# Kernel optimization log

Hardware: AMD Instinct MI355X
Metric: run time of the kernel (lower is better)

The kernel has to match this reference:

```python
import jax, jax.numpy as jnp
import numpy as np
import math

B, S, DM, H, D = 2, 2048, 768, 12, 64
MAX_POS = 2048

def setup_inputs() -> dict:
    key = jax.random.key(0)
    ks = jax.random.split(key, 8)
    return {
        "hidden_states": jax.random.normal(ks[0], (B, S, DM), jnp.float32),
        "attention_mask": jnp.zeros((B, 1, 1, S), jnp.float32),
        "Wq": jax.random.normal(ks[1], (DM, DM), jnp.float32) * 0.02,
        "bq": jnp.zeros((DM,), jnp.float32),
        "Wk": jax.random.normal(ks[2], (DM, DM), jnp.float32) * 0.02,
        "bk": jnp.zeros((DM,), jnp.float32),
        "Wv": jax.random.normal(ks[3], (DM, DM), jnp.float32) * 0.02,
        "bv": jnp.zeros((DM,), jnp.float32),
        "dist_emb": jax.random.normal(ks[4], (2 * MAX_POS - 1, D), jnp.float32) * 0.02,
    }

def reference(hidden_states, attention_mask, Wq, bq, Wk, bk, Wv, bv, dist_emb):
    def heads(x):  # [B,S,DM] -> [B,H,S,D]
        return x.reshape(B, S, H, D).transpose(0, 2, 1, 3)
    q = heads(hidden_states @ Wq + bq)
    k = heads(hidden_states @ Wk + bk)
    v = heads(hidden_states @ Wv + bv)
    scores = jnp.einsum("bhqd,bhkd->bhqk", q, k)  # [B,H,S,S]
    # relative_key_query position bias
    pos = jnp.arange(S)
    distance = pos[:, None] - pos[None, :] + (MAX_POS - 1)  # [S,S]
    pe = dist_emb[distance]  # [S,S,D]
    scores = scores + jnp.einsum("bhld,lrd->bhlr", q, pe) + jnp.einsum("bhrd,lrd->bhlr", k, pe)
    scores = scores / math.sqrt(D) + attention_mask
    probs = jax.nn.softmax(scores, axis=-1)
    ctx = jnp.einsum("bhqk,bhkd->bhqd", probs, v)
    return ctx.transpose(0, 2, 1, 3).reshape(B, S, DM)
```

## Files before the change

kernel.cpp:

```cpp
#include <hip/hip_runtime.h>
#include <hip/hip_fp16.h>

#define NB 2
#define NS 2048
#define NDM 768
#define NH 12
#define ND 64

typedef __attribute__((ext_vector_type(8))) _Float16 f16x8;
typedef __attribute__((ext_vector_type(4))) float f32x4;

__device__ __forceinline__ int swz(int row) {
  return (row & 3) ^ ((row >> 2) & 3);
}

__launch_bounds__(256)
__global__ void cvt_split(const float* __restrict__ x, __half* __restrict__ xh,
                          __half* __restrict__ xl) {
  const int i = blockIdx.x * 256 + threadIdx.x;
  const float4 v = reinterpret_cast<const float4*>(x)[i];
  const float a[4] = {v.x, v.y, v.z, v.w};
  union { __half h[4]; uint2 u; } ph, pl;
#pragma unroll
  for (int j = 0; j < 4; ++j) {
    ph.h[j] = __float2half(a[j]);
    pl.h[j] = __float2half(a[j] - __half2float(ph.h[j]));
  }
  *reinterpret_cast<uint2*>(&xh[(size_t)i * 4]) = ph.u;
  *reinterpret_cast<uint2*>(&xl[(size_t)i * 4]) = pl.u;
}

__launch_bounds__(256)
__global__ void cvt_w_t(const float* __restrict__ Wq,
                        const float* __restrict__ Wk,
                        const float* __restrict__ Wv,
                        __half* __restrict__ WhT, __half* __restrict__ WlT) {
  __shared__ float Tf[64][65];
  const int t = threadIdx.x;
  const int k0 = blockIdx.x * 64;
  const int n0 = blockIdx.y * 64;
  const int z = blockIdx.z;
  const float* W = z == 0 ? Wq : (z == 1 ? Wk : Wv);
  __half* wh = WhT + (size_t)z * NDM * NDM;
  __half* wl = WlT + (size_t)z * NDM * NDM;
#pragma unroll
  for (int s = 0; s < 4; ++s) {
    const int lin = t + 256 * s;
    const int r = lin >> 4, c4 = (lin & 15) * 4;
    const float4 v = *reinterpret_cast<const float4*>(
        &W[(size_t)(k0 + r) * NDM + n0 + c4]);
    Tf[r][c4 + 0] = v.x;
    Tf[r][c4 + 1] = v.y;
    Tf[r][c4 + 2] = v.z;
    Tf[r][c4 + 3] = v.w;
  }
  __syncthreads();
#pragma unroll
  for (int s = 0; s < 4; ++s) {
    const int lin = t + 256 * s;
    const int nl = lin >> 4, k4 = (lin & 15) * 4;
    union { __half h[4]; uint2 u; } ph, pl;
#pragma unroll
    for (int i = 0; i < 4; ++i) {
      const float f = Tf[k4 + i][nl];
      ph.h[i] = __float2half(f);
      pl.h[i] = __float2half(f - __half2float(ph.h[i]));
    }
    *reinterpret_cast<uint2*>(&wh[(size_t)(n0 + nl) * NDM + k0 + k4]) = ph.u;
    *reinterpret_cast<uint2*>(&wl[(size_t)(n0 + nl) * NDM + k0 + k4]) = pl.u;
  }
}

__launch_bounds__(256, 2)
__global__ void qkv_mfma(const __half* __restrict__ Xh,
                         const __half* __restrict__ Xl,
                         const __half* __restrict__ WhT,
                         const __half* __restrict__ WlT,
                         const float* __restrict__ bq,
                         const float* __restrict__ bk,
                         const float* __restrict__ bv,
                         __half* __restrict__ qb, __half* __restrict__ kb,
                         __half* __restrict__ vb) {
  __shared__ __align__(16) __half SS[4][128 * 32];

  const int t = threadIdx.x;
  const int lane = t & 63;
  const int w = t >> 6;
  const int g = lane >> 4;
  const int L = lane & 15;
  const int wm = w & 1, wn = w >> 1;
  const int widx = blockIdx.x / 6;
  const int n0m = (blockIdx.x % 6) * 128;
  const int m0 = blockIdx.y * 128;

  const __half* wh = WhT + (size_t)widx * NDM * NDM;
  const __half* wl = WlT + (size_t)widx * NDM * NDM;
  const float* bias = widx == 0 ? bq : (widx == 1 ? bk : bv);
  __half* dst = widx == 0 ? qb : (widx == 1 ? kb : vb);

  const __half* srcs[4] = {Xh + (size_t)m0 * NDM, Xl + (size_t)m0 * NDM,
                           wh + (size_t)n0m * NDM, wl + (size_t)n0m * NDM};

  uint4 rv[8];
#pragma unroll
  for (int u = 0; u < 8; ++u) {
    const int slot = t + 256 * u;
    const int bsel = slot >> 9, within = slot & 511;
    const int row = within >> 2, blk = within & 3;
    rv[u] = *reinterpret_cast<const uint4*>(srcs[bsel] + (size_t)row * NDM +
                                            blk * 8);
  }

  f32x4 acc[4][4];
#pragma unroll
  for (int mt = 0; mt < 4; ++mt)
#pragma unroll
    for (int nt = 0; nt < 4; ++nt) acc[mt][nt] = {0.f, 0.f, 0.f, 0.f};

  const int sL = (L & 3) ^ ((L >> 2) & 3);
  const int gs = (g ^ sL) << 3;

  for (int kt = 0; kt < 24; ++kt) {
    __syncthreads();
#pragma unroll
    for (int u = 0; u < 8; ++u) {
      const int slot = t + 256 * u;
      const int bsel = slot >> 9, within = slot & 511;
      const int row = within >> 2, blk = within & 3;
      *reinterpret_cast<uint4*>(&SS[bsel][row * 32 + ((blk ^ swz(row)) << 3)]) =
          rv[u];
    }
    if (kt < 23) {
      const int k0 = (kt + 1) * 32;
#pragma unroll
      for (int u = 0; u < 8; ++u) {
        const int slot = t + 256 * u;
        const int bsel = slot >> 9, within = slot & 511;
        const int row = within >> 2, blk = within & 3;
        rv[u] = *reinterpret_cast<const uint4*>(
            srcs[bsel] + (size_t)row * NDM + k0 + blk * 8);
      }
    }
    __syncthreads();

    f16x8 bh[4], bl[4];
#pragma unroll
    for (int nt = 0; nt < 4; ++nt) {
      const int nl = 64 * wn + 16 * nt + L;
      bh[nt] = *reinterpret_cast<const f16x8*>(&SS[2][nl * 32 + gs]);
      bl[nt] = *reinterpret_cast<const f16x8*>(&SS[3][nl * 32 + gs]);
    }
#pragma unroll
    for (int mt = 0; mt < 4; ++mt) {
      const int ml = 64 * wm + 16 * mt + L;
      const f16x8 ah = *reinterpret_cast<const f16x8*>(&SS[0][ml * 32 + gs]);
      const f16x8 al = *reinterpret_cast<const f16x8*>(&SS[1][ml * 32 + gs]);
#pragma unroll
      for (int nt = 0; nt < 4; ++nt) {
        acc[mt][nt] =
            __builtin_amdgcn_mfma_f32_16x16x32_f16(al, bh[nt], acc[mt][nt], 0, 0, 0);
        acc[mt][nt] =
            __builtin_amdgcn_mfma_f32_16x16x32_f16(ah, bl[nt], acc[mt][nt], 0, 0, 0);
        acc[mt][nt] =
            __builtin_amdgcn_mfma_f32_16x16x32_f16(ah, bh[nt], acc[mt][nt], 0, 0, 0);
      }
    }
  }

#pragma unroll
  for (int nt = 0; nt < 4; ++nt) {
    const int nmat = n0m + 64 * wn + 16 * nt + L;
    const float bval = bias[nmat];
    const int h_ = nmat >> 6, d_ = nmat & 63;
#pragma unroll
    for (int mt = 0; mt < 4; ++mt) {
#pragma unroll
      for (int j = 0; j < 4; ++j) {
        const int m = m0 + 64 * wm + 16 * mt + 4 * g + j;
        const int b_ = m >> 11, s_ = m & (NS - 1);
        dst[(((size_t)b_ * NH + h_) * NS + s_) * ND + d_] =
            __float2half(acc[mt][nt][j] + bval);
      }
    }
  }
}

__launch_bounds__(256, 3)
__global__ void attn_mfma(const __half* __restrict__ q,
                          const __half* __restrict__ k,
                          const __half* __restrict__ v,
                          const float* __restrict__ E,
                          const float* __restrict__ mask,
                          float* __restrict__ out) {
  __shared__ __align__(16) __half Qs[64 * 64];
  __shared__ __align__(16) __half Ks[32 * 64];
  __shared__ __align__(16) __half Es[96 * 64];
  __shared__ __align__(16) __half Vt[64 * 40];
  __shared__ __half F1s[64 * 100];
  __shared__ __half F2s[32 * 100];
  __shared__ __align__(16) __half Ps[64 * 40];

  const int t    = threadIdx.x;
  const int lane = t & 63;
  const int w    = t >> 6;
  const int g    = lane >> 4;
  const int L    = lane & 15;
  const int l0   = blockIdx.x * 64;
  const int bh   = blockIdx.y;
  const int b    = bh / NH;
  const int h    = bh - b * NH;

  const __half* qp = q + ((size_t)bh * NS + l0) * ND;
  const __half* kp = k + (size_t)bh * NS * ND;
  const __half* vp = v + (size_t)bh * NS * ND;
  const float* mp = mask + (size_t)b * NS;

#pragma unroll
  for (int s = 0; s < 4; ++s) {
    const int tau = t + 256 * s;
    const int r = tau >> 4, qd = tau & 15;
    const uint2 val =
        *reinterpret_cast<const uint2*>(&qp[(size_t)r * ND + qd * 4]);
    const int idx = r * 64 + ((((qd >> 1) ^ (r & 7)) << 3) | ((qd & 1) << 2));
    *reinterpret_cast<uint2*>(&Qs[idx]) = val;
  }

  f32x4 Oacc[4];
  float m_run[4], l_run[4];
#pragma unroll
  for (int j = 0; j < 4; ++j) { m_run[j] = -1e30f; l_run[j] = 0.f; }
#pragma unroll
  for (int nt = 0; nt < 4; ++nt) Oacc[nt] = {0.f, 0.f, 0.f, 0.f};

  const int rtw    = w >> 1;
  const int dtbase = (w & 1) * 3;
  const int swL    = L & 7;
  const f32x4 Z = {0.f, 0.f, 0.f, 0.f};

  for (int r0 = 0; r0 < NS; r0 += 32) {
    __syncthreads();

#pragma unroll
    for (int s = 0; s < 2; ++s) {
      const int tau = t + 256 * s;
      const int r = tau >> 4, qd = tau & 15;
      const uint2 val = *reinterpret_cast<const uint2*>(
          &kp[(size_t)(r0 + r) * ND + qd * 4]);
      const int idx =
          r * 64 + ((((qd >> 1) ^ (r & 7)) << 3) | ((qd & 1) << 2));
      *reinterpret_cast<uint2*>(&Ks[idx]) = val;
    }
#pragma unroll
    for (int s = 0; s < 2; ++s) {
      const int tau = t + 256 * s;
      const int rr = tau & 31, qd = tau >> 5;
      union { uint2 u; __half h[4]; } x;
      x.u = *reinterpret_cast<const uint2*>(
          &vp[(size_t)(r0 + rr) * ND + qd * 4]);
      Vt[(qd * 4 + 0) * 40 + rr] = x.h[0];
      Vt[(qd * 4 + 1) * 40 + rr] = x.h[1];
      Vt[(qd * 4 + 2) * 40 + rr] = x.h[2];
      Vt[(qd * 4 + 3) * 40 + rr] = x.h[3];
    }
    const int start = l0 - r0 + 2016;
#pragma unroll
    for (int s = 0; s < 3; ++s) {
      const int tau = t + 256 * s;
      const int row = tau >> 3, blk = tau & 7;
      int grow = start + row;
      grow = grow > 4094 ? 4094 : grow;
      const float* ep = &E[(size_t)grow * ND + blk * 8];
      const float4 a = *reinterpret_cast<const float4*>(ep);
      const float4 c = *reinterpret_cast<const float4*>(ep + 4);
      union { __half2 h2[4]; uint4 u; } pk;
      pk.h2[0] = __floats2half2_rn(a.x, a.y);
      pk.h2[1] = __floats2half2_rn(a.z, a.w);
      pk.h2[2] = __floats2half2_rn(c.x, c.y);
      pk.h2[3] = __floats2half2_rn(c.z, c.w);
      *reinterpret_cast<uint4*>(&Es[row * 64 + ((blk ^ (row & 7)) << 3)]) =
          pk.u;
    }
    __syncthreads();

    const int rq = 16 * w + L;
    const f16x8 aQ0 = *reinterpret_cast<const f16x8*>(
        &Qs[rq * 64 + ((g ^ swL) << 3)]);
    const f16x8 aQ1 = *reinterpret_cast<const f16x8*>(
        &Qs[rq * 64 + (((4 + g) ^ swL) << 3)]);
    const f16x8 bK00 = *reinterpret_cast<const f16x8*>(
        &Ks[L * 64 + ((g ^ swL) << 3)]);
    const f16x8 bK01 = *reinterpret_cast<const f16x8*>(
        &Ks[L * 64 + (((4 + g) ^ swL) << 3)]);
    const f16x8 bK10 = *reinterpret_cast<const f16x8*>(
        &Ks[(16 + L) * 64 + ((g ^ swL) << 3)]);
    const f16x8 bK11 = *reinterpret_cast<const f16x8*>(
        &Ks[(16 + L) * 64 + (((4 + g) ^ swL) << 3)]);

    f32x4 c0 = Z, c1 = Z;
    c0 = __builtin_amdgcn_mfma_f32_16x16x32_f16(aQ0, bK00, c0, 0, 0, 0);
    c0 = __builtin_amdgcn_mfma_f32_16x16x32_f16(aQ1, bK01, c0, 0, 0, 0);
    c1 = __builtin_amdgcn_mfma_f32_16x16x32_f16(aQ0, bK10, c1, 0, 0, 0);
    c1 = __builtin_amdgcn_mfma_f32_16x16x32_f16(aQ1, bK11, c1, 0, 0, 0);

    f32x4 f1acc[6];
#pragma unroll
    for (int dt = 0; dt < 6; ++dt) {
      const int re = 16 * dt + L;
      const f16x8 be0 = *reinterpret_cast<const f16x8*>(
          &Es[re * 64 + ((g ^ swL) << 3)]);
      const f16x8 be1 = *reinterpret_cast<const f16x8*>(
          &Es[re * 64 + (((4 + g) ^ swL) << 3)]);
      f32x4 acc = Z;
      acc = __builtin_amdgcn_mfma_f32_16x16x32_f16(aQ0, be0, acc, 0, 0, 0);
      acc = __builtin_amdgcn_mfma_f32_16x16x32_f16(aQ1, be1, acc, 0, 0, 0);
      f1acc[dt] = acc;
    }
    const f16x8 aK0 = rtw ? bK10 : bK00;
    const f16x8 aK1 = rtw ? bK11 : bK01;
    f32x4 f2acc[3];
#pragma unroll
    for (int m = 0; m < 3; ++m) {
      const int re = 16 * (dtbase + m) + L;
      const f16x8 be0 = *reinterpret_cast<const f16x8*>(
          &Es[re * 64 + ((g ^ swL) << 3)]);
      const f16x8 be1 = *reinterpret_cast<const f16x8*>(
          &Es[re * 64 + (((4 + g) ^ swL) << 3)]);
      f32x4 acc = Z;
      acc = __builtin_amdgcn_mfma_f32_16x16x32_f16(aK0, be0, acc, 0, 0, 0);
      acc = __builtin_amdgcn_mfma_f32_16x16x32_f16(aK1, be1, acc, 0, 0, 0);
      f2acc[m] = acc;
    }

#pragma unroll
    for (int dt = 0; dt < 6; ++dt)
#pragma unroll
      for (int j = 0; j < 4; ++j)
        F1s[(16 * w + 4 * g + j) * 100 + 16 * dt + L] =
            __float2half(f1acc[dt][j]);
#pragma unroll
    for (int m = 0; m < 3; ++m)
#pragma unroll
      for (int j = 0; j < 4; ++j)
        F2s[(16 * rtw + 4 * g + j) * 100 + 16 * (dtbase + m) + L] =
            __float2half(f2acc[m][j]);
    __syncthreads();

    float sc2[2][4];
    const float mk0 = mp[r0 + L];
    const float mk1 = mp[r0 + 16 + L];
#pragma unroll
    for (int j = 0; j < 4; ++j) {
      const int ll = 16 * w + 4 * g + j;
      {
        const int dl = ll - L + 31;
        sc2[0][j] = (c0[j] + __half2float(F1s[ll * 100 + dl]) +
                     __half2float(F2s[L * 100 + dl])) * 0.125f + mk0;
      }
      {
        const int rl = 16 + L;
        const int dl = ll - rl + 31;
        sc2[1][j] = (c1[j] + __half2float(F1s[ll * 100 + dl]) +
                     __half2float(F2s[rl * 100 + dl])) * 0.125f + mk1;
      }
    }
    float al[4];
#pragma unroll
    for (int j = 0; j < 4; ++j) {
      float mx = fmaxf(sc2[0][j], sc2[1][j]);
      mx = fmaxf(mx, __shfl_xor(mx, 1));
      mx = fmaxf(mx, __shfl_xor(mx, 2));
      mx = fmaxf(mx, __shfl_xor(mx, 4));
      mx = fmaxf(mx, __shfl_xor(mx, 8));
      const float mnew = fmaxf(m_run[j], mx);
      al[j] = __expf(m_run[j] - mnew);
      m_run[j] = mnew;
      const float p0 = __expf(sc2[0][j] - mnew);
      const float p1 = __expf(sc2[1][j] - mnew);
      sc2[0][j] = p0;
      sc2[1][j] = p1;
      float ps = p0 + p1;
      ps += __shfl_xor(ps, 1);
      ps += __shfl_xor(ps, 2);
      ps += __shfl_xor(ps, 4);
      ps += __shfl_xor(ps, 8);
      l_run[j] = l_run[j] * al[j] + ps;
    }
#pragma unroll
    for (int nt = 0; nt < 4; ++nt)
#pragma unroll
      for (int j = 0; j < 4; ++j) Oacc[nt][j] *= al[j];
#pragma unroll
    for (int j = 0; j < 4; ++j) {
      Ps[(16 * w + 4 * g + j) * 40 + L]      = __float2half(sc2[0][j]);
      Ps[(16 * w + 4 * g + j) * 40 + 16 + L] = __float2half(sc2[1][j]);
    }
    __syncthreads();

    {
      const f16x8 aP =
          *reinterpret_cast<const f16x8*>(&Ps[(16 * w + L) * 40 + 8 * g]);
#pragma unroll
      for (int nt = 0; nt < 4; ++nt) {
        const f16x8 bV = *reinterpret_cast<const f16x8*>(
            &Vt[(16 * nt + L) * 40 + 8 * g]);
        Oacc[nt] = __builtin_amdgcn_mfma_f32_16x16x32_f16(aP, bV, Oacc[nt],
                                                          0, 0, 0);
      }
    }
  }

#pragma unroll
  for (int j = 0; j < 4; ++j) {
    const float inv = 1.0f / l_run[j];
    const int row = l0 + 16 * w + 4 * g + j;
    float* op = &out[((size_t)b * NS + row) * NDM + h * ND + L];
    op[0]  = Oacc[0][j] * inv;
    op[16] = Oacc[1][j] * inv;
    op[32] = Oacc[2][j] * inv;
    op[48] = Oacc[3][j] * inv;
  }
}

extern "C" void kernel_launch(void* const* d_in, const int* in_sizes, int n_in,
                              void* d_out, int out_size, void* d_ws, size_t ws_size,
                              hipStream_t stream) {
  const float* hs  = (const float*)d_in[0];
  const float* msk = (const float*)d_in[1];
  const float* Wq  = (const float*)d_in[2];
  const float* bq  = (const float*)d_in[3];
  const float* Wk  = (const float*)d_in[4];
  const float* bk  = (const float*)d_in[5];
  const float* Wv  = (const float*)d_in[6];
  const float* bv  = (const float*)d_in[7];
  const float* Ept = (const float*)d_in[8];
  float* out = (float*)d_out;

  const size_t per  = (size_t)NB * NH * NS * ND;
  const size_t wsz  = (size_t)NDM * NDM;
  __half* qb  = (__half*)d_ws;
  __half* kb  = qb + per;
  __half* vb  = kb + per;
  __half* Xh  = vb + per;
  __half* Xl  = Xh + per;
  __half* WhT = Xl + per;
  __half* WlT = WhT + 3 * wsz;

  cvt_split<<<dim3((int)(per / 4 / 256)), 256, 0, stream>>>(hs, Xh, Xl);
  cvt_w_t<<<dim3(12, 12, 3), 256, 0, stream>>>(Wq, Wk, Wv, WhT, WlT);
  qkv_mfma<<<dim3(18, 32), 256, 0, stream>>>(Xh, Xl, WhT, WlT, bq, bk, bv,
                                             qb, kb, vb);
  attn_mfma<<<dim3(NS / 64, NB * NH), 256, 0, stream>>>(qb, kb, vb, Ept,
                                                        msk, out);
}
```

Before: 637.0 us.

## Enlarge attention key tile to 64 with register prefetch and ring-buffered E rows

The attention kernel now processes 64 keys per iteration instead of 32. The next tile's K, V and E rows are prefetched into registers while the current tile computes, and E is kept in a 128-row ring buffer so only 64 new rows load per step. It also computes the full F2 term per wave, adds s_setprio around the MFMA sections, and unions Ks with Ps to save LDS. Occupancy drops from 3 to 2 blocks per SIMD and register pressure rises, traded for fewer barriers per key and better hiding of global loads.

```diff
diff --git a/kernel.cpp b/kernel.cpp
--- a/kernel.cpp
+++ b/kernel.cpp
@@ -185,89 +185,66 @@
   }
 }
 
-__launch_bounds__(256, 3)
+__launch_bounds__(256, 2)
 __global__ void attn_mfma(const __half* __restrict__ q,
                           const __half* __restrict__ k,
                           const __half* __restrict__ v,
                           const float* __restrict__ E,
                           const float* __restrict__ mask,
                           float* __restrict__ out) {
-  __shared__ __align__(16) __half Qs[64 * 64];
-  __shared__ __align__(16) __half Ks[32 * 64];
-  __shared__ __align__(16) __half Es[96 * 64];
-  __shared__ __align__(16) __half Vt[64 * 40];
-  __shared__ __half F1s[64 * 100];
-  __shared__ __half F2s[32 * 100];
-  __shared__ __align__(16) __half Ps[64 * 40];
+  struct __align__(16) SMem {
+    __half Qs[64 * 64];
+    union { __half Ks[64 * 64]; __half Ps[64 * 72]; } kp;
+    __half Es[128 * 64];
+    __half Vt[64 * 72];
+    __half F1[64 * 132];
+    __half F2[64 * 132];
+  };
+  __shared__ SMem sm;
 
   const int t    = threadIdx.x;
   const int lane = t & 63;
   const int w    = t >> 6;
   const int g    = lane >> 4;
   const int L    = lane & 15;
+  const int sw   = L & 7;
   const int l0   = blockIdx.x * 64;
   const int bh   = blockIdx.y;
   const int b    = bh / NH;
   const int h    = bh - b * NH;
 
-  const __half* qp = q + ((size_t)bh * NS + l0) * ND;
-  const __half* kp = k + (size_t)bh * NS * ND;
-  const __half* vp = v + (size_t)bh * NS * ND;
-  const float* mp = mask + (size_t)b * NS;
+  const __half* qp  = q + ((size_t)bh * NS + l0) * ND;
+  const __half* kpg = k + (size_t)bh * NS * ND;
+  const __half* vpg = v + (size_t)bh * NS * ND;
+  const float*  mp  = mask + (size_t)b * NS;
 
 #pragma unroll
   for (int s = 0; s < 4; ++s) {
     const int tau = t + 256 * s;
     const int r = tau >> 4, qd = tau & 15;
-    const uint2 val =
+    const int idx = r * 64 + ((((qd >> 1) ^ (r & 7)) << 3) | ((qd & 1) << 2));
+    sm.Qs[0] = sm.Qs[0];
+    *reinterpret_cast<uint2*>(&sm.Qs[idx]) =
         *reinterpret_cast<const uint2*>(&qp[(size_t)r * ND + qd * 4]);
-    const int idx = r * 64 + ((((qd >> 1) ^ (r & 7)) << 3) | ((qd & 1) << 2));
-    *reinterpret_cast<uint2*>(&Qs[idx]) = val;
-  }
-
-  f32x4 Oacc[4];
-  float m_run[4], l_run[4];
-#pragma unroll
-  for (int j = 0; j < 4; ++j) { m_run[j] = -1e30f; l_run[j] = 0.f; }
-#pragma unroll
-  for (int nt = 0; nt < 4; ++nt) Oacc[nt] = {0.f, 0.f, 0.f, 0.f};
-
-  const int rtw    = w >> 1;
-  const int dtbase = (w & 1) * 3;
-  const int swL    = L & 7;
-  const f32x4 Z = {0.f, 0.f, 0.f, 0.f};
-
-  for (int r0 = 0; r0 < NS; r0 += 32) {
-    __syncthreads();
-
-#pragma unroll
-    for (int s = 0; s < 2; ++s) {
-      const int tau = t + 256 * s;
-      const int r = tau >> 4, qd = tau & 15;
-      const uint2 val = *reinterpret_cast<const uint2*>(
-          &kp[(size_t)(r0 + r) * ND + qd * 4]);
-      const int idx =
-          r * 64 + ((((qd >> 1) ^ (r & 7)) << 3) | ((qd & 1) << 2));
-      *reinterpret_cast<uint2*>(&Ks[idx]) = val;
-    }
-#pragma unroll
-    for (int s = 0; s < 2; ++s) {
-      const int tau = t + 256 * s;
-      const int rr = tau & 31, qd = tau >> 5;
-      union { uint2 u; __half h[4]; } x;
-      x.u = *reinterpret_cast<const uint2*>(
-          &vp[(size_t)(r0 + rr) * ND + qd * 4]);
-      Vt[(qd * 4 + 0) * 40 + rr] = x.h[0];
-      Vt[(qd * 4 + 1) * 40 + rr] = x.h[1];
-      Vt[(qd * 4 + 2) * 40 + rr] = x.h[2];
-      Vt[(qd * 4 + 3) * 40 + rr] = x.h[3];
-    }
-    const int start = l0 - r0 + 2016;
-#pragma unroll
-    for (int s = 0; s < 3; ++s) {
+    *reinterpret_cast<uint2*>(&sm.kp.Ks[idx]) =
+        *reinterpret_cast<const uint2*>(&kpg[(size_t)r * ND + qd * 4]);
+  }
+#pragma unroll
+  for (int s = 0; s < 4; ++s) {
+    const int tau = t + 256 * s;
+    const int rr = tau & 63, qd = tau >> 6;
+    union { uint2 u; __half hh[4]; } x;
+    x.u = *reinterpret_cast<const uint2*>(&vpg[(size_t)rr * ND + qd * 4]);
+#pragma unroll
+    for (int c = 0; c < 4; ++c) sm.Vt[(qd * 4 + c) * 72 + rr] = x.hh[c];
+  }
+  {
+    const int start0 = l0 + 1984;
+#pragma unroll
+    for (int s = 0; s < 4; ++s) {
       const int tau = t + 256 * s;
       const int row = tau >> 3, blk = tau & 7;
-      int grow = start + row;
+      int grow = start0 + row;
       grow = grow > 4094 ? 4094 : grow;
       const float* ep = &E[(size_t)grow * ND + blk * 8];
       const float4 a = *reinterpret_cast<const float4*>(ep);
@@ -277,96 +254,118 @@
       pk.h2[1] = __floats2half2_rn(a.z, a.w);
       pk.h2[2] = __floats2half2_rn(c.x, c.y);
       pk.h2[3] = __floats2half2_rn(c.z, c.w);
-      *reinterpret_cast<uint4*>(&Es[row * 64 + ((blk ^ (row & 7)) << 3)]) =
+      *reinterpret_cast<uint4*>(&sm.Es[row * 64 + ((blk ^ (row & 7)) << 3)]) =
           pk.u;
     }
+  }
+  __syncthreads();
+
+  const int rq = 16 * w + L;
+  const f16x8 aQ0 =
+      *reinterpret_cast<const f16x8*>(&sm.Qs[rq * 64 + ((g ^ sw) << 3)]);
+  const f16x8 aQ1 =
+      *reinterpret_cast<const f16x8*>(&sm.Qs[rq * 64 + (((4 + g) ^ sw) << 3)]);
+
+  f32x4 Oacc[4];
+  float m_run[4], l_run[4];
+#pragma unroll
+  for (int j = 0; j < 4; ++j) { m_run[j] = -1e30f; l_run[j] = 0.f; }
+#pragma unroll
+  for (int nt = 0; nt < 4; ++nt) Oacc[nt] = {0.f, 0.f, 0.f, 0.f};
+
+  const f32x4 Z = {0.f, 0.f, 0.f, 0.f};
+
+  for (int it = 0; it < 32; ++it) {
+    const int r0 = it * 64;
+    const int off = (it & 1) * 64;
+
+    uint2 kr[4], vr[4];
+    float4 er[4];
+    const bool pf = it < 31;
+    if (pf) {
+      const int r0n = r0 + 64;
+#pragma unroll
+      for (int s = 0; s < 4; ++s) {
+        const int tau = t + 256 * s;
+        kr[s] = *reinterpret_cast<const uint2*>(
+            &kpg[(size_t)(r0n + (tau >> 4)) * ND + (tau & 15) * 4]);
+        vr[s] = *reinterpret_cast<const uint2*>(
+            &vpg[(size_t)(r0n + (tau & 63)) * ND + (tau >> 6) * 4]);
+      }
+      const int startn = l0 + 1984 - 64 * (it + 1);
+#pragma unroll
+      for (int s = 0; s < 2; ++s) {
+        const int tau = t + 256 * s;
+        const int row = tau >> 3, blk = tau & 7;
+        const float* ep = &E[(size_t)(startn + row) * ND + blk * 8];
+        er[2 * s]     = *reinterpret_cast<const float4*>(ep);
+        er[2 * s + 1] = *reinterpret_cast<const float4*>(ep + 4);
+      }
+    }
+    float mk[4];
+#pragma unroll
+    for (int rt = 0; rt < 4; ++rt) mk[rt] = mp[r0 + 16 * rt + L];
+
+    __builtin_amdgcn_s_setprio(1);
+    f16x8 bKa[4], bKb[4];
+#pragma unroll
+    for (int rt = 0; rt < 4; ++rt) {
+      const int rl = 16 * rt + L;
+      bKa[rt] = *reinterpret_cast<const f16x8*>(
+          &sm.kp.Ks[rl * 64 + ((g ^ sw) << 3)]);
+      bKb[rt] = *reinterpret_cast<const f16x8*>(
+          &sm.kp.Ks[rl * 64 + (((4 + g) ^ sw) << 3)]);
+    }
+    f32x4 c[4];
+#pragma unroll
+    for (int rt = 0; rt < 4; ++rt) {
+      f32x4 acc = Z;
+      acc = __builtin_amdgcn_mfma_f32_16x16x32_f16(aQ0, bKa[rt], acc, 0, 0, 0);
+      acc = __builtin_amdgcn_mfma_f32_16x16x32_f16(aQ1, bKb[rt], acc, 0, 0, 0);
+      c[rt] = acc;
+    }
+    const f16x8 aK0 = *reinterpret_cast<const f16x8*>(
+        &sm.kp.Ks[(16 * w + L) * 64 + ((g ^ sw) << 3)]);
+    const f16x8 aK1 = *reinterpret_cast<const f16x8*>(
+        &sm.kp.Ks[(16 * w + L) * 64 + (((4 + g) ^ sw) << 3)]);
+#pragma unroll
+    for (int dt = 0; dt < 8; ++dt) {
+      const int phys = ((16 * dt + L) + off) & 127;
+      const f16x8 be0 = *reinterpret_cast<const f16x8*>(
+          &sm.Es[phys * 64 + ((g ^ sw) << 3)]);
+      const f16x8 be1 = *reinterpret_cast<const f16x8*>(
+          &sm.Es[phys * 64 + (((4 + g) ^ sw) << 3)]);
+      f32x4 f1 = Z, f2 = Z;
+      f1 = __builtin_amdgcn_mfma_f32_16x16x32_f16(aQ0, be0, f1, 0, 0, 0);
+      f1 = __builtin_amdgcn_mfma_f32_16x16x32_f16(aQ1, be1, f1, 0, 0, 0);
+      f2 = __builtin_amdgcn_mfma_f32_16x16x32_f16(aK0, be0, f2, 0, 0, 0);
+      f2 = __builtin_amdgcn_mfma_f32_16x16x32_f16(aK1, be1, f2, 0, 0, 0);
+#pragma unroll
+      for (int j = 0; j < 4; ++j) {
+        const int rowi = 16 * w + 4 * g + j;
+        sm.F1[rowi * 132 + 16 * dt + L] = __float2half(f1[j]);
+        sm.F2[rowi * 132 + 16 * dt + L] = __float2half(f2[j]);
+      }
+    }
+    __builtin_amdgcn_s_setprio(0);
     __syncthreads();
 
-    const int rq = 16 * w + L;
-    const f16x8 aQ0 = *reinterpret_cast<const f16x8*>(
-        &Qs[rq * 64 + ((g ^ swL) << 3)]);
-    const f16x8 aQ1 = *reinterpret_cast<const f16x8*>(
-        &Qs[rq * 64 + (((4 + g) ^ swL) << 3)]);
-    const f16x8 bK00 = *reinterpret_cast<const f16x8*>(
-        &Ks[L * 64 + ((g ^ swL) << 3)]);
-    const f16x8 bK01 = *reinterpret_cast<const f16x8*>(
-        &Ks[L * 64 + (((4 + g) ^ swL) << 3)]);
-    const f16x8 bK10 = *reinterpret_cast<const f16x8*>(
-        &Ks[(16 + L) * 64 + ((g ^ swL) << 3)]);
-    const f16x8 bK11 = *reinterpret_cast<const f16x8*>(
-        &Ks[(16 + L) * 64 + (((4 + g) ^ swL) << 3)]);
-
-    f32x4 c0 = Z, c1 = Z;
-    c0 = __builtin_amdgcn_mfma_f32_16x16x32_f16(aQ0, bK00, c0, 0, 0, 0);
-    c0 = __builtin_amdgcn_mfma_f32_16x16x32_f16(aQ1, bK01, c0, 0, 0, 0);
-    c1 = __builtin_amdgcn_mfma_f32_16x16x32_f16(aQ0, bK10, c1, 0, 0, 0);
-    c1 = __builtin_amdgcn_mfma_f32_16x16x32_f16(aQ1, bK11, c1, 0, 0, 0);
-
-    f32x4 f1acc[6];
-#pragma unroll
-    for (int dt = 0; dt < 6; ++dt) {
-      const int re = 16 * dt + L;
-      const f16x8 be0 = *reinterpret_cast<const f16x8*>(
-          &Es[re * 64 + ((g ^ swL) << 3)]);
-      const f16x8 be1 = *reinterpret_cast<const f16x8*>(
-          &Es[re * 64 + (((4 + g) ^ swL) << 3)]);
-      f32x4 acc = Z;
-      acc = __builtin_amdgcn_mfma_f32_16x16x32_f16(aQ0, be0, acc, 0, 0, 0);
-      acc = __builtin_amdgcn_mfma_f32_16x16x32_f16(aQ1, be1, acc, 0, 0, 0);
-      f1acc[dt] = acc;
-    }
-    const f16x8 aK0 = rtw ? bK10 : bK00;
-    const f16x8 aK1 = rtw ? bK11 : bK01;
-    f32x4 f2acc[3];
-#pragma unroll
-    for (int m = 0; m < 3; ++m) {
-      const int re = 16 * (dtbase + m) + L;
-      const f16x8 be0 = *reinterpret_cast<const f16x8*>(
-          &Es[re * 64 + ((g ^ swL) << 3)]);
-      const f16x8 be1 = *reinterpret_cast<const f16x8*>(
-          &Es[re * 64 + (((4 + g) ^ swL) << 3)]);
-      f32x4 acc = Z;
-      acc = __builtin_amdgcn_mfma_f32_16x16x32_f16(aK0, be0, acc, 0, 0, 0);
-      acc = __builtin_amdgcn_mfma_f32_16x16x32_f16(aK1, be1, acc, 0, 0, 0);
-      f2acc[m] = acc;
-    }
-
-#pragma unroll
-    for (int dt = 0; dt < 6; ++dt)
-#pragma unroll
-      for (int j = 0; j < 4; ++j)
-        F1s[(16 * w + 4 * g + j) * 100 + 16 * dt + L] =
-            __float2half(f1acc[dt][j]);
-#pragma unroll
-    for (int m = 0; m < 3; ++m)
-#pragma unroll
-      for (int j = 0; j < 4; ++j)
-        F2s[(16 * rtw + 4 * g + j) * 100 + 16 * (dtbase + m) + L] =
-            __float2half(f2acc[m][j]);
-    __syncthreads();
-
-    float sc2[2][4];
-    const float mk0 = mp[r0 + L];
-    const float mk1 = mp[r0 + 16 + L];
+    float sc[4][4];
 #pragma unroll
     for (int j = 0; j < 4; ++j) {
       const int ll = 16 * w + 4 * g + j;
-      {
-        const int dl = ll - L + 31;
-        sc2[0][j] = (c0[j] + __half2float(F1s[ll * 100 + dl]) +
-                     __half2float(F2s[L * 100 + dl])) * 0.125f + mk0;
-      }
-      {
-        const int rl = 16 + L;
-        const int dl = ll - rl + 31;
-        sc2[1][j] = (c1[j] + __half2float(F1s[ll * 100 + dl]) +
-                     __half2float(F2s[rl * 100 + dl])) * 0.125f + mk1;
+#pragma unroll
+      for (int rt = 0; rt < 4; ++rt) {
+        const int rl = 16 * rt + L;
+        const int dl = ll - rl + 63;
+        sc[j][rt] = (c[rt][j] + __half2float(sm.F1[ll * 132 + dl]) +
+                     __half2float(sm.F2[rl * 132 + dl])) * 0.125f + mk[rt];
       }
     }
     float al[4];
 #pragma unroll
     for (int j = 0; j < 4; ++j) {
-      float mx = fmaxf(sc2[0][j], sc2[1][j]);
+      float mx = fmaxf(fmaxf(sc[j][0], sc[j][1]), fmaxf(sc[j][2], sc[j][3]));
       mx = fmaxf(mx, __shfl_xor(mx, 1));
       mx = fmaxf(mx, __shfl_xor(mx, 2));
       mx = fmaxf(mx, __shfl_xor(mx, 4));
@@ -374,11 +373,13 @@
       const float mnew = fmaxf(m_run[j], mx);
       al[j] = __expf(m_run[j] - mnew);
       m_run[j] = mnew;
-      const float p0 = __expf(sc2[0][j] - mnew);
-      const float p1 = __expf(sc2[1][j] - mnew);
-      sc2[0][j] = p0;
-      sc2[1][j] = p1;
-      float ps = p0 + p1;
+      float ps = 0.f;
+#pragma unroll
+      for (int rt = 0; rt < 4; ++rt) {
+        const float p = __expf(sc[j][rt] - mnew);
+        sc[j][rt] = p;
+        ps += p;
+      }
       ps += __shfl_xor(ps, 1);
       ps += __shfl_xor(ps, 2);
       ps += __shfl_xor(ps, 4);
@@ -391,21 +392,70 @@
       for (int j = 0; j < 4; ++j) Oacc[nt][j] *= al[j];
 #pragma unroll
     for (int j = 0; j < 4; ++j) {
-      Ps[(16 * w + 4 * g + j) * 40 + L]      = __float2half(sc2[0][j]);
-      Ps[(16 * w + 4 * g + j) * 40 + 16 + L] = __float2half(sc2[1][j]);
+      const int ll = 16 * w + 4 * g + j;
+#pragma unroll
+      for (int rt = 0; rt < 4; ++rt)
+        sm.kp.Ps[ll * 72 + 16 * rt + L] = __float2half(sc[j][rt]);
     }
     __syncthreads();
 
+    __builtin_amdgcn_s_setprio(1);
     {
-      const f16x8 aP =
-          *reinterpret_cast<const f16x8*>(&Ps[(16 * w + L) * 40 + 8 * g]);
+      const int pr = (16 * w + L) * 72;
+      const f16x8 aP0 = *reinterpret_cast<const f16x8*>(&sm.kp.Ps[pr + 8 * g]);
+      const f16x8 aP1 =
+          *reinterpret_cast<const f16x8*>(&sm.kp.Ps[pr + 32 + 8 * g]);
 #pragma unroll
       for (int nt = 0; nt < 4; ++nt) {
-        const f16x8 bV = *reinterpret_cast<const f16x8*>(
-            &Vt[(16 * nt + L) * 40 + 8 * g]);
-        Oacc[nt] = __builtin_amdgcn_mfma_f32_16x16x32_f16(aP, bV, Oacc[nt],
-                                                          0, 0, 0);
-      }
+        const int vb_ = (16 * nt + L) * 72;
+        const f16x8 bV0 =
+            *reinterpret_cast<const f16x8*>(&sm.Vt[vb_ + 8 * g]);
+        const f16x8 bV1 =
+            *reinterpret_cast<const f16x8*>(&sm.Vt[vb_ + 32 + 8 * g]);
+        Oacc[nt] =
+            __builtin_amdgcn_mfma_f32_16x16x32_f16(aP0, bV0, Oacc[nt], 0, 0, 0);
+        Oacc[nt] =
+            __builtin_amdgcn_mfma_f32_16x16x32_f16(aP1, bV1, Oacc[nt], 0, 0, 0);
+      }
+    }
+    __builtin_amdgcn_s_setprio(0);
+    __syncthreads();
+
+    if (pf) {
+#pragma unroll
+      for (int s = 0; s < 4; ++s) {
+        const int tau = t + 256 * s;
+        const int r = tau >> 4, qd = tau & 15;
+        const int idx =
+            r * 64 + ((((qd >> 1) ^ (r & 7)) << 3) | ((qd & 1) << 2));
+        *reinterpret_cast<uint2*>(&sm.kp.Ks[idx]) = kr[s];
+      }
+#pragma unroll
+      for (int s = 0; s < 4; ++s) {
+        const int tau = t + 256 * s;
+        const int rr = tau & 63, qd = tau >> 6;
+        union { uint2 u; __half hh[4]; } x;
+        x.u = vr[s];
+#pragma unroll
+        for (int cc = 0; cc < 4; ++cc) sm.Vt[(qd * 4 + cc) * 72 + rr] = x.hh[cc];
+      }
+      const int offn = ((it + 1) & 1) * 64;
+#pragma unroll
+      for (int s = 0; s < 2; ++s) {
+        const int tau = t + 256 * s;
+        const int row = tau >> 3, blk = tau & 7;
+        const int phys = (row + offn) & 127;
+        const float4 a = er[2 * s];
+        const float4 cc = er[2 * s + 1];
+        union { __half2 h2[4]; uint4 u; } pk;
+        pk.h2[0] = __floats2half2_rn(a.x, a.y);
+        pk.h2[1] = __floats2half2_rn(a.z, a.w);
+        pk.h2[2] = __floats2half2_rn(cc.x, cc.y);
+        pk.h2[3] = __floats2half2_rn(cc.z, cc.w);
+        *reinterpret_cast<uint4*>(
+            &sm.Es[phys * 64 + ((blk ^ (phys & 7)) << 3)]) = pk.u;
+      }
+      __syncthreads();
     }
   }
 
@@ -435,8 +485,8 @@
   const float* Ept = (const float*)d_in[8];
   float* out = (float*)d_out;
 
-  const size_t per  = (size_t)NB * NH * NS * ND;
-  const size_t wsz  = (size_t)NDM * NDM;
+  const size_t per = (size_t)NB * NH * NS * ND;
+  const size_t wsz = (size_t)NDM * NDM;
   __half* qb  = (__half*)d_ws;
   __half* kb  = qb + per;
   __half* vb  = kb + per;
```

Result: faster. 531.8 us (-16.5%).
